# Kernel tuning notes

Hardware: AMD Instinct MI355X
Metric: run time of the kernel (lower is better)

Reference implementation:

```python
import jax, jax.numpy as jnp
import numpy as np

B, DIM, HID, K, G, MID = 1024, 384, 64, 8, 48, 128
EPS = 1e-06


def _gaussian_8x8():
    t = jnp.arange(K, dtype=jnp.float32) - 3.5
    g = jnp.exp(-(t[:, None] ** 2 + t[None, :] ** 2) / (2.0 * 2.0 ** 2))
    return g / g.sum()


def setup_inputs() -> dict:
    key = jax.random.key(0)
    ks = jax.random.split(key, 16)
    inp = {
        "x": jax.random.normal(ks[0], (B, DIM), dtype=jnp.float32),
        "W": jax.random.normal(ks[1], (DIM, HID), dtype=jnp.float32) * 0.02,
        "b": jax.random.normal(ks[2], (DIM, HID), dtype=jnp.float32) * 0.02,
        "patch_weight": _gaussian_8x8(),  # learnable 8x8, softmaxed in forward
        "pair_w1": jax.random.normal(ks[3], (G, G), dtype=jnp.float32) * 0.02,
        "pair_b1": jax.random.normal(ks[4], (G, G), dtype=jnp.float32) * 0.02,
        "pair_w2": jax.random.normal(ks[5], (G, G), dtype=jnp.float32) * 0.02,
        "pair_b2": jax.random.normal(ks[6], (G, G), dtype=jnp.float32) * 0.02,
        # nn.Linear(G, DIM)
        "proj_w": jax.random.normal(ks[7], (DIM, G), dtype=jnp.float32) * (1.0 / np.sqrt(G)),
        "proj_b": jax.random.normal(ks[8], (DIM,), dtype=jnp.float32) * 0.02,
        # nn.Linear(HID, MID)
        "down_w": jax.random.normal(ks[9], (MID, HID), dtype=jnp.float32) * (1.0 / np.sqrt(HID)),
        "down_b": jax.random.normal(ks[10], (MID,), dtype=jnp.float32) * 0.02,
        # nn.Linear(MID, HID)
        "up_w": jax.random.normal(ks[11], (HID, MID), dtype=jnp.float32) * (1.0 / np.sqrt(MID)),
        "up_b": jax.random.normal(ks[12], (HID,), dtype=jnp.float32) * 0.02,
    }
    return inp


def _leaky(v):
    return jnp.where(v >= 0, v, 0.01 * v)


def reference(x, W, b, patch_weight, pair_w1, pair_b1, pair_w2, pair_b2,
              proj_w, proj_b, down_w, down_b, up_w, up_b):
    # scale / inverse-bias GELU features: (B, DIM, HID)
    s = x[:, :, None]
    inv = 1.0 / (jnp.abs(s) + EPS)
    H = jax.nn.gelu(s * W[None] + inv * b[None], approximate=False)
    # Gram matrix over hidden dim: (B, DIM, DIM)
    P = jnp.einsum('bik,bjk->bij', H, H)
    # learnable gaussian patch pooling (softmax over flattened 8x8 weights)
    w = jax.nn.softmax(patch_weight.reshape(-1)).reshape(K, K)
    Pg = jnp.einsum('bgkhl,kl->bgh', P.reshape(-1, G, K, G, K), w)  # (B, G, G)
    # two elementwise gated leaky layers
    Pg = _leaky(Pg * pair_w1[None] + pair_b1[None])
    Pg = _leaky(Pg * pair_w2[None] + pair_b2[None])
    # softmax + nonlinear row reduction -> (B, G)
    row_soft = jax.nn.softmax(Pg, axis=-1)
    row_weights = (1.0 / (1.0 + row_soft ** 2)).sum(axis=-1)
    # project 48 -> 384, scale rows of H
    scales = row_weights @ proj_w.T + proj_b  # (B, DIM)
    H = H * scales[:, :, None]
    # tiny MLP on hidden dim
    z = _leaky(H @ down_w.T + down_b)
    z = _leaky(z @ up_w.T + up_b)
    return z
```

## Files before the change

kernel.cpp:

```cpp
#include <hip/hip_runtime.h>


#define EPSF 1e-6f

typedef __attribute__((ext_vector_type(8))) short bf16x8;
typedef __attribute__((ext_vector_type(4))) float f32x4;
typedef __attribute__((ext_vector_type(4))) unsigned short u16x4;

__device__ __forceinline__ unsigned short f2bf(float f) {
    union { float f; unsigned int u; } v; v.f = f;
    unsigned int r = v.u + 0x7fffu + ((v.u >> 16) & 1u);
    return (unsigned short)(r >> 16);
}
__device__ __forceinline__ float bf2f(unsigned short h) {
    union { unsigned int u; float f; } v; v.u = ((unsigned int)h) << 16;
    return v.f;
}
__device__ __forceinline__ float leaky(float v) { return fmaxf(v, 0.01f * v); }
__device__ __forceinline__ int key8(int r) { return (r ^ (r >> 3)) & 7; }
__device__ __forceinline__ float gelu_f(float u) {
    float t = u * (1.5957691216f + 0.0713548163f * (u * u));
    float e = __expf(t);
    float r = __builtin_amdgcn_rcpf(e + 1.0f);
    return fmaf(-u, r, u);
}

__global__ void prep(const float* __restrict__ proj_w,
                     const float* __restrict__ down_w,
                     const float* __restrict__ up_w,
                     float* __restrict__ ws) {
    int idx = blockIdx.x * blockDim.x + threadIdx.x;
    unsigned short* wb = (unsigned short*)(ws + 18432);
    if (idx < 18432) {
        int i = idx / 48, g = idx % 48;
        ws[g * 384 + i] = proj_w[idx];
    } else if (idx < 26624) {
        int k = idx - 18432;
        wb[k] = f2bf(down_w[k]);
    } else if (idx < 34816) {
        int k = idx - 26624;
        wb[8192 + k] = f2bf(up_w[k]);
    }
}

__global__ __launch_bounds__(512, 4) void fused_main(
    const float* __restrict__ x,
    const float* __restrict__ W,
    const float* __restrict__ bb,
    const float* __restrict__ patch_weight,
    const float* __restrict__ pw1, const float* __restrict__ pb1,
    const float* __restrict__ pw2, const float* __restrict__ pb2,
    const float* __restrict__ proj_b,
    const float* __restrict__ down_b,
    const float* __restrict__ up_b,
    const float* __restrict__ ws,
    float* __restrict__ out)
{
    __shared__ __align__(16) unsigned short sH[24576];
    __shared__ __align__(16) unsigned short sRB[12288];
    __shared__ float sw[64];
    __shared__ float srw[48];
    __shared__ float sScale[384];
    __shared__ float sDb[128];
    __shared__ float sUb[64];

    const int t = threadIdx.x;
    const int b = blockIdx.x;
    const int wv = t >> 6, lane = t & 63, q = lane >> 4, r = lane & 15;
    const float* projT = ws;
    const unsigned short* dwB = (const unsigned short*)(ws + 18432);
    const unsigned short* uwB = dwB + 8192;
    unsigned short* sM  = sRB;
    float* sPg = (float*)sRB;
    unsigned short* sZ1 = sRB;

    if (t < 64) {
        float p = patch_weight[t];
        float m = p;
        for (int o = 32; o > 0; o >>= 1) m = fmaxf(m, __shfl_xor(m, o));
        float e = __expf(p - m);
        float s = e;
        for (int o = 32; o > 0; o >>= 1) s += __shfl_xor(s, o);
        sw[t] = e * __builtin_amdgcn_rcpf(s);
    }

    for (int j = 0; j < 12; ++j) {
        int idx4 = j * 512 + t;
        int base = idx4 * 4;
        int i = base >> 6, c0 = base & 63;
        float4 w4 = ((const float4*)W)[idx4];
        float4 b4 = ((const float4*)bb)[idx4];
        float xi  = x[b * 384 + i];
        float inv = __builtin_amdgcn_rcpf(fabsf(xi) + EPSF);
        u16x4 hv;
        hv[0] = f2bf(gelu_f(fmaf(xi, w4.x, inv * b4.x)));
        hv[1] = f2bf(gelu_f(fmaf(xi, w4.y, inv * b4.y)));
        hv[2] = f2bf(gelu_f(fmaf(xi, w4.z, inv * b4.z)));
        hv[3] = f2bf(gelu_f(fmaf(xi, w4.w, inv * b4.w)));
        int cb = c0 >> 3, cc = c0 & 7;
        *(u16x4*)&sH[i * 64 + ((cb ^ key8(i)) << 3) + cc] = hv;
    }
    __syncthreads();

    f32x4 pacc  = {0.f, 0.f, 0.f, 0.f};
    f32x4 pacc8 = {0.f, 0.f, 0.f, 0.f};
    for (int hc = 0; hc < 2; ++hc) {
        if (t < 384) {
            const int cb = t & 3, lq = (t >> 2) & 1, g = t >> 3;
            float acc[4][8];
            #pragma unroll
            for (int a = 0; a < 4; ++a)
                #pragma unroll
                for (int cc = 0; cc < 8; ++cc) acc[a][cc] = 0.0f;
            #pragma unroll
            for (int k = 0; k < 8; ++k) {
                int i = g * 8 + k;
                int cbh = hc * 4 + cb;
                bf16x8 hv = *(const bf16x8*)&sH[i * 64 + ((cbh ^ key8(i)) << 3)];
                f32x4 w4 = *(const f32x4*)&sw[k * 8 + lq * 4];
                float hf[8];
                #pragma unroll
                for (int cc = 0; cc < 8; ++cc) hf[cc] = bf2f((unsigned short)hv[cc]);
                #pragma unroll
                for (int a = 0; a < 4; ++a)
                    #pragma unroll
                    for (int cc = 0; cc < 8; ++cc)
                        acc[a][cc] = fmaf(w4[a], hf[cc], acc[a][cc]);
            }
            #pragma unroll
            for (int a = 0; a < 4; ++a) {
                int l = lq * 4 + a;
                int cbl = l * 4 + cb;
                int cbs = (cbl & 24) | ((cbl ^ key8(g)) & 7);
                bf16x8 mv;
                #pragma unroll
                for (int cc = 0; cc < 8; ++cc) mv[cc] = (short)f2bf(acc[a][cc]);
                *(bf16x8*)&sM[g * 256 + (cbs << 3)] = mv;
            }
        } else if (hc == 0) {
            int tt = t - 384;
            if (tt < 128) sDb[tt] = down_b[tt];
            if (tt < 64)  sUb[tt] = up_b[tt];
        }
        __syncthreads();
        {
            const int tg = wv / 3, th = wv % 3;
            #pragma unroll
            for (int ks = 0; ks < 8; ++ks) {
                int g = tg * 16 + r;
                int cbl = ks * 4 + q;
                int cbs = (cbl & 24) | ((cbl ^ key8(g)) & 7);
                bf16x8 av = *(const bf16x8*)&sM[g * 256 + (cbs << 3)];
                int i = (th * 16 + r) * 8 + ks;
                int cbh = hc * 4 + q;
                bf16x8 bv = *(const bf16x8*)&sH[i * 64 + ((cbh ^ key8(i)) << 3)];
                pacc = __builtin_amdgcn_mfma_f32_16x16x32_bf16(av, bv, pacc, 0, 0, 0);
            }
            if (wv == 7) {
                #pragma unroll
                for (int ks = 0; ks < 8; ++ks) {
                    int g = 32 + r;
                    int cbl = ks * 4 + q;
                    int cbs = (cbl & 24) | ((cbl ^ key8(g)) & 7);
                    bf16x8 av = *(const bf16x8*)&sM[g * 256 + (cbs << 3)];
                    int i = (32 + r) * 8 + ks;
                    int cbh = hc * 4 + q;
                    bf16x8 bv = *(const bf16x8*)&sH[i * 64 + ((cbh ^ key8(i)) << 3)];
                    pacc8 = __builtin_amdgcn_mfma_f32_16x16x32_bf16(av, bv, pacc8, 0, 0, 0);
                }
            }
        }
        __syncthreads();
    }

    {
        const int tg = wv / 3, th = wv % 3;
        #pragma unroll
        for (int reg = 0; reg < 4; ++reg) {
            int g = tg * 16 + q * 4 + reg;
            int h = th * 16 + r;
            int idx = g * 48 + h;
            float v = pacc[reg];
            v = leaky(fmaf(v, pw1[idx], pb1[idx]));
            v = leaky(fmaf(v, pw2[idx], pb2[idx]));
            sPg[g * 49 + h] = v;
        }
        if (wv == 7) {
            #pragma unroll
            for (int reg = 0; reg < 4; ++reg) {
                int g = 32 + q * 4 + reg;
                int h = 32 + r;
                int idx = g * 48 + h;
                float v = pacc8[reg];
                v = leaky(fmaf(v, pw1[idx], pb1[idx]));
                v = leaky(fmaf(v, pw2[idx], pb2[idx]));
                sPg[g * 49 + h] = v;
            }
        }
    }
    __syncthreads();

    if (wv < 6) {
        #pragma unroll
        for (int it = 0; it < 2; ++it) {
            int row = wv * 8 + it * 4 + (lane >> 4);
            int idx = lane & 15;
            const float* pr = &sPg[row * 49 + idx * 3];
            float v0 = pr[0], v1 = pr[1], v2 = pr[2];
            float m = fmaxf(v0, fmaxf(v1, v2));
            #pragma unroll
            for (int o = 8; o > 0; o >>= 1) m = fmaxf(m, __shfl_xor(m, o));
            float e0 = __expf(v0 - m), e1 = __expf(v1 - m), e2 = __expf(v2 - m);
            float s = e0 + e1 + e2;
            #pragma unroll
            for (int o = 8; o > 0; o >>= 1) s += __shfl_xor(s, o);
            float rs = __builtin_amdgcn_rcpf(s);
            float p0 = e0 * rs, p1 = e1 * rs, p2 = e2 * rs;
            float rw = __builtin_amdgcn_rcpf(fmaf(p0, p0, 1.0f))
                     + __builtin_amdgcn_rcpf(fmaf(p1, p1, 1.0f))
                     + __builtin_amdgcn_rcpf(fmaf(p2, p2, 1.0f));
            #pragma unroll
            for (int o = 8; o > 0; o >>= 1) rw += __shfl_xor(rw, o);
            if (idx == 0) srw[row] = rw;
        }
    }
    __syncthreads();

    #pragma unroll 1
    for (int rt = 0; rt < 4; ++rt) {
        const int r0 = rt * 96;
        if (rt == 0 && t < 384) {
            float s = proj_b[t];
            #pragma unroll 4
            for (int g = 0; g < 48; ++g) s = fmaf(srw[g], projT[g * 384 + t], s);
            sScale[t] = s;
        }
        f32x4 zacc[6];
        #pragma unroll
        for (int a = 0; a < 6; ++a) zacc[a] = (f32x4){0.f, 0.f, 0.f, 0.f};
        #pragma unroll
        for (int ks = 0; ks < 2; ++ks) {
            int cb = ks * 4 + q;
            int n = wv * 16 + r;
            bf16x8 bv = *(const bf16x8*)&dwB[n * 64 + cb * 8];
            #pragma unroll
            for (int a = 0; a < 6; ++a) {
                int i = r0 + a * 16 + r;
                bf16x8 av = *(const bf16x8*)&sH[i * 64 + ((cb ^ key8(i)) << 3)];
                zacc[a] = __builtin_amdgcn_mfma_f32_16x16x32_bf16(av, bv, zacc[a], 0, 0, 0);
            }
        }
        __syncthreads();
        #pragma unroll
        for (int a = 0; a < 6; ++a) {
            #pragma unroll
            for (int reg = 0; reg < 4; ++reg) {
                int rl = a * 16 + q * 4 + reg;
                int m = wv * 16 + r;
                float v = leaky(fmaf(zacc[a][reg], sScale[r0 + rl], sDb[m]));
                int cb2 = m >> 3;
                int cbs2 = (cb2 & 8) | ((cb2 ^ key8(rl)) & 7);
                sZ1[rl * 128 + (cbs2 << 3) + (m & 7)] = f2bf(v);
            }
        }
        __syncthreads();
        {
            const int grp = wv >> 2, nt = wv & 3;
            f32x4 oacc[3];
            #pragma unroll
            for (int a = 0; a < 3; ++a) oacc[a] = (f32x4){0.f, 0.f, 0.f, 0.f};
            #pragma unroll
            for (int ks = 0; ks < 4; ++ks) {
                int cb = ks * 4 + q;
                int p = nt * 16 + r;
                bf16x8 bv = *(const bf16x8*)&uwB[p * 128 + cb * 8];
                #pragma unroll
                for (int a = 0; a < 3; ++a) {
                    int rl = (grp * 3 + a) * 16 + r;
                    int cbsA = (cb & 8) | ((cb ^ key8(rl)) & 7);
                    bf16x8 av = *(const bf16x8*)&sZ1[rl * 128 + (cbsA << 3)];
                    oacc[a] = __builtin_amdgcn_mfma_f32_16x16x32_bf16(av, bv, oacc[a], 0, 0, 0);
                }
            }
            #pragma unroll
            for (int a = 0; a < 3; ++a) {
                #pragma unroll
                for (int reg = 0; reg < 4; ++reg) {
                    int i = r0 + (grp * 3 + a) * 16 + q * 4 + reg;
                    int cp = nt * 16 + r;
                    out[(b * 384 + i) * 64 + cp] = leaky(oacc[a][reg] + sUb[cp]);
                }
            }
        }
    }
}

extern "C" void kernel_launch(void* const* d_in, const int* in_sizes, int n_in,
                              void* d_out, int out_size, void* d_ws, size_t ws_size,
                              hipStream_t stream) {
    const float* x      = (const float*)d_in[0];
    const float* W      = (const float*)d_in[1];
    const float* bb     = (const float*)d_in[2];
    const float* pw     = (const float*)d_in[3];
    const float* pw1    = (const float*)d_in[4];
    const float* pb1    = (const float*)d_in[5];
    const float* pw2    = (const float*)d_in[6];
    const float* pb2    = (const float*)d_in[7];
    const float* proj_w = (const float*)d_in[8];
    const float* proj_b = (const float*)d_in[9];
    const float* down_w = (const float*)d_in[10];
    const float* down_b = (const float*)d_in[11];
    const float* up_w   = (const float*)d_in[12];
    const float* up_b   = (const float*)d_in[13];
    float* out = (float*)d_out;
    float* ws  = (float*)d_ws;

    prep<<<(34816 + 255) / 256, 256, 0, stream>>>(proj_w, down_w, up_w, ws);
    fused_main<<<1024, 512, 0, stream>>>(x, W, bb, pw, pw1, pb1, pw2, pb2,
                                         proj_b, down_b, up_b, ws, out);
}
```

Baseline: 188.2 us.

## Split fused kernel into Gram/scales kernel and separate row-tiled FFN kernel

Splits the single fused kernel in two. The first kernel computes the pooled Gram path and writes per-row scales to workspace. A second kernel with 4096 blocks recomputes the GELU features for a 96-row tile and runs the down/up MLP, using less shared memory so that more blocks fit per CU. This targets the serial FFN tail in the fused kernel and the low occupancy caused by its large LDS footprint. The cost is recomputing H, an extra launch, and a global round trip for the scales.

Measured after the change: 213.6 us. 13.5% more time.

```diff
diff --git a/kernel.cpp b/kernel.cpp
--- a/kernel.cpp
+++ b/kernel.cpp
@@ -43,7 +43,7 @@
     }
 }
 
-__global__ __launch_bounds__(512, 4) void fused_main(
+__global__ __launch_bounds__(512, 4) void pg_scales(
     const float* __restrict__ x,
     const float* __restrict__ W,
     const float* __restrict__ bb,
@@ -51,28 +51,20 @@
     const float* __restrict__ pw1, const float* __restrict__ pb1,
     const float* __restrict__ pw2, const float* __restrict__ pb2,
     const float* __restrict__ proj_b,
-    const float* __restrict__ down_b,
-    const float* __restrict__ up_b,
-    const float* __restrict__ ws,
-    float* __restrict__ out)
+    float* __restrict__ ws)
 {
     __shared__ __align__(16) unsigned short sH[24576];
     __shared__ __align__(16) unsigned short sRB[12288];
     __shared__ float sw[64];
     __shared__ float srw[48];
-    __shared__ float sScale[384];
-    __shared__ float sDb[128];
-    __shared__ float sUb[64];
 
     const int t = threadIdx.x;
     const int b = blockIdx.x;
     const int wv = t >> 6, lane = t & 63, q = lane >> 4, r = lane & 15;
     const float* projT = ws;
-    const unsigned short* dwB = (const unsigned short*)(ws + 18432);
-    const unsigned short* uwB = dwB + 8192;
+    float* scales_g = ws + 26624;
     unsigned short* sM  = sRB;
     float* sPg = (float*)sRB;
-    unsigned short* sZ1 = sRB;
 
     if (t < 64) {
         float p = patch_weight[t];
@@ -137,10 +129,6 @@
                 for (int cc = 0; cc < 8; ++cc) mv[cc] = (short)f2bf(acc[a][cc]);
                 *(bf16x8*)&sM[g * 256 + (cbs << 3)] = mv;
             }
-        } else if (hc == 0) {
-            int tt = t - 384;
-            if (tt < 128) sDb[tt] = down_b[tt];
-            if (tt < 64)  sUb[tt] = up_b[tt];
         }
         __syncthreads();
         {
@@ -226,70 +214,127 @@
     }
     __syncthreads();
 
-    #pragma unroll 1
-    for (int rt = 0; rt < 4; ++rt) {
-        const int r0 = rt * 96;
-        if (rt == 0 && t < 384) {
-            float s = proj_b[t];
-            #pragma unroll 4
-            for (int g = 0; g < 48; ++g) s = fmaf(srw[g], projT[g * 384 + t], s);
-            sScale[t] = s;
-        }
-        f32x4 zacc[6];
-        #pragma unroll
-        for (int a = 0; a < 6; ++a) zacc[a] = (f32x4){0.f, 0.f, 0.f, 0.f};
-        #pragma unroll
-        for (int ks = 0; ks < 2; ++ks) {
-            int cb = ks * 4 + q;
-            int n = wv * 16 + r;
+    if (t < 384) {
+        float s = proj_b[t];
+        #pragma unroll 4
+        for (int g = 0; g < 48; ++g) s = fmaf(srw[g], projT[g * 384 + t], s);
+        scales_g[b * 384 + t] = s;
+    }
+}
+
+__global__ __launch_bounds__(512, 8) void ffn(
+    const float* __restrict__ x,
+    const float* __restrict__ W,
+    const float* __restrict__ bb,
+    const float* __restrict__ down_b,
+    const float* __restrict__ up_b,
+    const float* __restrict__ ws,
+    float* __restrict__ out)
+{
+    __shared__ __align__(16) unsigned short sHc[6144];
+    __shared__ __align__(16) unsigned short sZ1[12288];
+    __shared__ float sSc[96];
+    __shared__ float sDb[128];
+    __shared__ float sUb[64];
+
+    const int t = threadIdx.x;
+    const int bid = blockIdx.x;
+    const int b = bid >> 2, rt = bid & 3, r0 = rt * 96;
+    const int wv = t >> 6, lane = t & 63, q = lane >> 4, r = lane & 15;
+    const unsigned short* dwB = (const unsigned short*)(ws + 18432);
+    const unsigned short* uwB = dwB + 8192;
+    const float* scales_g = ws + 26624;
+
+    #pragma unroll
+    for (int j = 0; j < 3; ++j) {
+        int idx4 = j * 512 + t;
+        int ir = idx4 >> 4;
+        int i  = r0 + ir;
+        int f4 = idx4 & 15;
+        float4 w4 = ((const float4*)W)[i * 16 + f4];
+        float4 b4 = ((const float4*)bb)[i * 16 + f4];
+        float xi  = x[b * 384 + i];
+        float inv = __builtin_amdgcn_rcpf(fabsf(xi) + EPSF);
+        u16x4 hv;
+        hv[0] = f2bf(gelu_f(fmaf(xi, w4.x, inv * b4.x)));
+        hv[1] = f2bf(gelu_f(fmaf(xi, w4.y, inv * b4.y)));
+        hv[2] = f2bf(gelu_f(fmaf(xi, w4.z, inv * b4.z)));
+        hv[3] = f2bf(gelu_f(fmaf(xi, w4.w, inv * b4.w)));
+        int c0 = f4 * 4;
+        int cb = c0 >> 3, cc = c0 & 7;
+        *(u16x4*)&sHc[ir * 64 + ((cb ^ key8(ir)) << 3) + cc] = hv;
+    }
+    if (t < 128) sDb[t] = down_b[t];
+    else if (t < 192) sUb[t - 128] = up_b[t - 128];
+    else if (t >= 416) sSc[t - 416] = scales_g[b * 384 + r0 + (t - 416)];
+    __syncthreads();
+
+    const int mg = wv >> 2, ng = wv & 3;
+    f32x4 zacc[3][2];
+    #pragma unroll
+    for (int a = 0; a < 3; ++a)
+        #pragma unroll
+        for (int e = 0; e < 2; ++e) zacc[a][e] = (f32x4){0.f, 0.f, 0.f, 0.f};
+    #pragma unroll
+    for (int ks = 0; ks < 2; ++ks) {
+        int cb = ks * 4 + q;
+        bf16x8 af[3];
+        #pragma unroll
+        for (int a = 0; a < 3; ++a) {
+            int ir = (mg * 3 + a) * 16 + r;
+            af[a] = *(const bf16x8*)&sHc[ir * 64 + ((cb ^ key8(ir)) << 3)];
+        }
+        #pragma unroll
+        for (int e = 0; e < 2; ++e) {
+            int n = (ng * 2 + e) * 16 + r;
             bf16x8 bv = *(const bf16x8*)&dwB[n * 64 + cb * 8];
             #pragma unroll
-            for (int a = 0; a < 6; ++a) {
-                int i = r0 + a * 16 + r;
-                bf16x8 av = *(const bf16x8*)&sH[i * 64 + ((cb ^ key8(i)) << 3)];
-                zacc[a] = __builtin_amdgcn_mfma_f32_16x16x32_bf16(av, bv, zacc[a], 0, 0, 0);
-            }
-        }
-        __syncthreads();
-        #pragma unroll
-        for (int a = 0; a < 6; ++a) {
+            for (int a = 0; a < 3; ++a)
+                zacc[a][e] = __builtin_amdgcn_mfma_f32_16x16x32_bf16(af[a], bv, zacc[a][e], 0, 0, 0);
+        }
+    }
+    #pragma unroll
+    for (int a = 0; a < 3; ++a) {
+        #pragma unroll
+        for (int e = 0; e < 2; ++e) {
             #pragma unroll
             for (int reg = 0; reg < 4; ++reg) {
-                int rl = a * 16 + q * 4 + reg;
-                int m = wv * 16 + r;
-                float v = leaky(fmaf(zacc[a][reg], sScale[r0 + rl], sDb[m]));
+                int rl = (mg * 3 + a) * 16 + q * 4 + reg;
+                int m = (ng * 2 + e) * 16 + r;
+                float v = leaky(fmaf(zacc[a][e][reg], sSc[rl], sDb[m]));
                 int cb2 = m >> 3;
                 int cbs2 = (cb2 & 8) | ((cb2 ^ key8(rl)) & 7);
                 sZ1[rl * 128 + (cbs2 << 3) + (m & 7)] = f2bf(v);
             }
         }
-        __syncthreads();
-        {
-            const int grp = wv >> 2, nt = wv & 3;
-            f32x4 oacc[3];
-            #pragma unroll
-            for (int a = 0; a < 3; ++a) oacc[a] = (f32x4){0.f, 0.f, 0.f, 0.f};
-            #pragma unroll
-            for (int ks = 0; ks < 4; ++ks) {
-                int cb = ks * 4 + q;
-                int p = nt * 16 + r;
-                bf16x8 bv = *(const bf16x8*)&uwB[p * 128 + cb * 8];
-                #pragma unroll
-                for (int a = 0; a < 3; ++a) {
-                    int rl = (grp * 3 + a) * 16 + r;
-                    int cbsA = (cb & 8) | ((cb ^ key8(rl)) & 7);
-                    bf16x8 av = *(const bf16x8*)&sZ1[rl * 128 + (cbsA << 3)];
-                    oacc[a] = __builtin_amdgcn_mfma_f32_16x16x32_bf16(av, bv, oacc[a], 0, 0, 0);
-                }
-            }
+    }
+    __syncthreads();
+
+    {
+        const int grp = wv >> 2, nt = wv & 3;
+        f32x4 oacc[3];
+        #pragma unroll
+        for (int a = 0; a < 3; ++a) oacc[a] = (f32x4){0.f, 0.f, 0.f, 0.f};
+        #pragma unroll
+        for (int ks = 0; ks < 4; ++ks) {
+            int cb = ks * 4 + q;
+            int p = nt * 16 + r;
+            bf16x8 bv = *(const bf16x8*)&uwB[p * 128 + cb * 8];
             #pragma unroll
             for (int a = 0; a < 3; ++a) {
-                #pragma unroll
-                for (int reg = 0; reg < 4; ++reg) {
-                    int i = r0 + (grp * 3 + a) * 16 + q * 4 + reg;
-                    int cp = nt * 16 + r;
-                    out[(b * 384 + i) * 64 + cp] = leaky(oacc[a][reg] + sUb[cp]);
-                }
+                int rl = (grp * 3 + a) * 16 + r;
+                int cbsA = (cb & 8) | ((cb ^ key8(rl)) & 7);
+                bf16x8 av = *(const bf16x8*)&sZ1[rl * 128 + (cbsA << 3)];
+                oacc[a] = __builtin_amdgcn_mfma_f32_16x16x32_bf16(av, bv, oacc[a], 0, 0, 0);
+            }
+        }
+        #pragma unroll
+        for (int a = 0; a < 3; ++a) {
+            #pragma unroll
+            for (int reg = 0; reg < 4; ++reg) {
+                int i = r0 + (grp * 3 + a) * 16 + q * 4 + reg;
+                int cp = nt * 16 + r;
+                out[(b * 384 + i) * 64 + cp] = leaky(oacc[a][reg] + sUb[cp]);
             }
         }
     }
@@ -316,6 +361,7 @@
     float* ws  = (float*)d_ws;
 
     prep<<<(34816 + 255) / 256, 256, 0, stream>>>(proj_w, down_w, up_w, ws);
-    fused_main<<<1024, 512, 0, stream>>>(x, W, bb, pw, pw1, pb1, pw2, pb2,
-                                         proj_b, down_b, up_b, ws, out);
-}
+    pg_scales<<<1024, 512, 0, stream>>>(x, W, bb, pw, pw1, pb1, pw2, pb2,
+                                        proj_b, ws);
+    ffn<<<4096, 512, 0, stream>>>(x, W, bb, down_b, up_b, ws, out);
+}
```
